# Kernel tuning notes

Hardware: AMD Instinct MI355X
Metric: run time of the kernel (lower is better)

## Reference

```python
import jax, jax.numpy as jnp
import numpy as np

K = 128
NITER = 10


def _sq_dist(x, c):
    x2 = jnp.sum(x * x, axis=1, keepdims=True)          # [N,1]
    c2 = jnp.sum(c * c, axis=1)                          # [K]
    return x2 + c2[None, :] - 2.0 * (x @ c.T)


def _kmeans(x, key):
    N, D = x.shape
    idx = jax.random.permutation(key, N)[:K]             # torch.randperm(N)[:K]
    c0 = x[idx]

    def step(c, _):
        cl = jnp.argmin(_sq_dist(x, c), axis=1)          # nearest assignment [N]
        counts = jax.ops.segment_sum(jnp.ones((N,), x.dtype), cl, num_segments=K)  # bincount
        sums = jax.ops.segment_sum(x, cl, num_segments=K)                          # [K,D] (vectorized over D)
        # c = sums / counts; NaN (empty cluster, 0/0) -> 0, matching c[isnan(c)]=0
        c_new = jnp.where(counts[:, None] > 0, sums / jnp.maximum(counts, 1.0)[:, None], 0.0)
        return c_new, None

    c, _ = jax.lax.scan(step, c0, None, length=NITER)
    return c


def setup_inputs() -> dict:
    key = jax.random.key(0)
    x = jax.random.normal(key, (500000, 64), dtype=jnp.float32)
    return {"x": x}


def reference(x):
    # KMeans runs on x.detach(); forward output has no grad path through centroids
    centroids = _kmeans(jax.lax.stop_gradient(x), jax.random.key(42))
    distances = _sq_dist(x, centroids)                   # [N, K]
    # Faithful to normalize_distance: distances.sum(1, keepdim=True)[0] indexes
    # ROW 0 of the [N,1] row-sums -> a single scalar broadcast to all rows.
    denom = jnp.sum(distances[0])
    probs = 1.0 - distances / denom
    return probs
```

## Files before the change

kernel.cpp:

```cpp
#include <hip/hip_runtime.h>
#include <cstdint>
#include <cstddef>

#define NPTS 500000
#define DIM 64
#define KC 128
#define KM_ITERS 10
#define NGROUPS (NPTS / 32)
#define NITERS ((NGROUPS + 3) / 4)

typedef __bf16 bf16x8 __attribute__((ext_vector_type(8)));
typedef float f32x4 __attribute__((ext_vector_type(4)));

__device__ __forceinline__ float wave_reduce_add(float v) {
#pragma unroll
  for (int off = 32; off > 0; off >>= 1) v += __shfl_xor(v, off, 64);
  return v;
}

__device__ __forceinline__ bf16x8 cvt8(float4 a, float4 b) {
  bf16x8 r;
  r[0] = (__bf16)a.x; r[1] = (__bf16)a.y; r[2] = (__bf16)a.z; r[3] = (__bf16)a.w;
  r[4] = (__bf16)b.x; r[5] = (__bf16)b.y; r[6] = (__bf16)b.z; r[7] = (__bf16)b.w;
  return r;
}

__global__ void k_cvt(const float* __restrict__ x, bf16x8* __restrict__ xb8) {
  int n = NPTS * DIM / 8;
  for (int i = blockIdx.x * 256 + threadIdx.x; i < n; i += gridDim.x * 256) {
    const float4* xp = (const float4*)(x + (size_t)i * 8);
    xb8[i] = cvt8(xp[0], xp[1]);
  }
}

__global__ void k_initc(const float* __restrict__ x, float* __restrict__ cent,
                        float* __restrict__ c2, float* __restrict__ sums,
                        float* __restrict__ cnts) {
  int k = blockIdx.x, d = threadIdx.x;
  long src = (long)k * 3891 + 7;
  float v = x[src * DIM + d];
  cent[k * DIM + d] = v;
  sums[k * DIM + d] = 0.f;
  float s = wave_reduce_add(v * v);
  if (d == 0) { c2[k] = s; cnts[k] = 0.f; }
}

__global__ void k_update(const float* __restrict__ sums, const float* __restrict__ cnts,
                         float* __restrict__ cent, float* __restrict__ c2,
                         float* __restrict__ sums_z, float* __restrict__ cnts_z) {
  int k = blockIdx.x, d = threadIdx.x;
  float c = cnts[k];
  float v = (c > 0.f) ? (sums[k * DIM + d] / c) : 0.f;
  cent[k * DIM + d] = v;
  sums_z[k * DIM + d] = 0.f;
  float s = wave_reduce_add(v * v);
  if (d == 0) { c2[k] = s; cnts_z[k] = 0.f; }
}

#define DIST_H(V0, V1, MK)                                                     \
  {                                                                            \
    f32x4 acc[8];                                                              \
    _Pragma("unroll") for (int tt = 0; tt < 8; tt++)                           \
      acc[tt] = (f32x4){c2h[tt * 4 + 0], c2h[tt * 4 + 1],                      \
                        c2h[tt * 4 + 2], c2h[tt * 4 + 3]};                     \
    _Pragma("unroll") for (int tt = 0; tt < 8; tt++)                           \
      acc[tt] = __builtin_amdgcn_mfma_f32_16x16x32_bf16(afr0[tt], V0, acc[tt], 0, 0, 0); \
    _Pragma("unroll") for (int tt = 0; tt < 8; tt++)                           \
      acc[tt] = __builtin_amdgcn_mfma_f32_16x16x32_bf16(afr1[tt], V1, acc[tt], 0, 0, 0); \
    float maxv = -3.4e38f; int mk = 0;                                         \
    _Pragma("unroll") for (int tt = 0; tt < 8; tt++)                           \
      _Pragma("unroll") for (int r = 0; r < 4; r++) {                          \
        float a = acc[tt][r];                                                  \
        int k = tt * 16 + grp * 4 + r;                                         \
        if (a > maxv) { maxv = a; mk = k; }                                    \
      }                                                                        \
    _Pragma("unroll") for (int off = 16; off <= 32; off <<= 1) {               \
      float ov = __shfl_xor(maxv, off, 64);                                    \
      int ok = __shfl_xor(mk, off, 64);                                        \
      if (ov > maxv || (ov == maxv && ok < mk)) { maxv = ov; mk = ok; }        \
    }                                                                          \
    MK = mk;                                                                   \
  }

__global__ __launch_bounds__(256, 2)
void k_assign(const __bf16* __restrict__ xb, const float* __restrict__ cent,
              const float* __restrict__ c2, float* __restrict__ sums,
              float* __restrict__ cnts) {
  __shared__ char xT[4][5120];
  __shared__ int sm[4][32];
  __shared__ float lc[KC];

  const int lane = threadIdx.x & 63;
  const int wid = threadIdx.x >> 6;
  const int col = lane & 15;
  const int grp = lane >> 4;

  bf16x8 afr0[8], afr1[8];
  float c2h[32];
#pragma unroll
  for (int t = 0; t < 8; t++) {
    const float* cp = cent + (size_t)(t * 16 + col) * DIM;
    float4 f0 = *(const float4*)(cp + grp * 8);
    float4 f1 = *(const float4*)(cp + grp * 8 + 4);
    afr0[t] = cvt8(f0, f1);
    float4 g0 = *(const float4*)(cp + 32 + grp * 8);
    float4 g1 = *(const float4*)(cp + 32 + grp * 8 + 4);
    afr1[t] = cvt8(g0, g1);
#pragma unroll
    for (int r = 0; r < 4; r++) c2h[t * 4 + r] = -0.5f * c2[t * 16 + grp * 4 + r];
  }
#pragma unroll
  for (int t = 0; t < 8; t++) asm volatile("" : "+v"(afr0[t]), "+v"(afr1[t]));
#pragma unroll
  for (int i = 0; i < 32; i++) asm volatile("" : "+v"(c2h[i]));

  for (int i = threadIdx.x; i < KC; i += 256) lc[i] = 0.f;
  __syncthreads();

  f32x4 accs[8];
#pragma unroll
  for (int i = 0; i < 8; i++) accs[i] = (f32x4){0.f, 0.f, 0.f, 0.f};

  const int kbase = wid * 32;

  for (int it = blockIdx.x; it < NITERS; it += gridDim.x) {
    int g = it * 4 + wid;
    int mk0 = -1, mk1 = -1;
    if (g < NGROUPS) {
      int n0 = g * 32;
      const bf16x8* xr0 = (const bf16x8*)(xb + (size_t)(n0 + col) * DIM + grp * 8);
      const bf16x8* xr1 = (const bf16x8*)(xb + (size_t)(n0 + 16 + col) * DIM + grp * 8);
      bf16x8 v0a = xr0[0], v1a = xr0[4];
      bf16x8 v0b = xr1[0], v1b = xr1[4];

      char* xTw = xT[wid];
      {
        int slotb = ((((0 << 1) | (col >> 3)) ^ grp) & 3) * 16 + (col & 7) * 2;
#pragma unroll
        for (int j = 0; j < 8; j++) {
          *(__bf16*)(xTw + (grp * 8 + j) * 80 + slotb) = v0a[j];
          *(__bf16*)(xTw + (32 + grp * 8 + j) * 80 + slotb) = v1a[j];
        }
      }
      {
        int slotb = ((((1 << 1) | (col >> 3)) ^ grp) & 3) * 16 + (col & 7) * 2;
#pragma unroll
        for (int j = 0; j < 8; j++) {
          *(__bf16*)(xTw + (grp * 8 + j) * 80 + slotb) = v0b[j];
          *(__bf16*)(xTw + (32 + grp * 8 + j) * 80 + slotb) = v1b[j];
        }
      }

      DIST_H(v0a, v1a, mk0);
      DIST_H(v0b, v1b, mk1);

      if (grp == 0) {
        atomicAdd(&lc[mk0], 1.f);
        atomicAdd(&lc[mk1], 1.f);
      }
    }
    if (grp == 0) { sm[wid][col] = mk0; sm[wid][16 + col] = mk1; }
    __syncthreads();

#pragma unroll
    for (int G = 0; G < 4; G++) {
      const int* smG = sm[G];
      int4 mlo = *(const int4*)&smG[grp * 8];
      int4 mhi = *(const int4*)&smG[grp * 8 + 4];
      const char* xTg = xT[G];
      bf16x8 xf0, xf1, xf2, xf3;
      { int d = col;      int s = (grp ^ ((d >> 3) & 3)) & 3; xf0 = *(const bf16x8*)(xTg + d * 80 + s * 16); }
      { int d = 16 + col; int s = (grp ^ ((d >> 3) & 3)) & 3; xf1 = *(const bf16x8*)(xTg + d * 80 + s * 16); }
      { int d = 32 + col; int s = (grp ^ ((d >> 3) & 3)) & 3; xf2 = *(const bf16x8*)(xTg + d * 80 + s * 16); }
      { int d = 48 + col; int s = (grp ^ ((d >> 3) & 3)) & 3; xf3 = *(const bf16x8*)(xTg + d * 80 + s * 16); }
      int m0 = mlo.x, m1 = mlo.y, m2 = mlo.z, m3 = mlo.w;
      int m4 = mhi.x, m5 = mhi.y, m6 = mhi.z, m7 = mhi.w;
#pragma unroll
      for (int tt2 = 0; tt2 < 2; tt2++) {
        int c = kbase + tt2 * 16 + col;
        union { unsigned u[4]; bf16x8 v; } oh;
        oh.u[0] = (m0 == c ? 0x3F80u : 0u) | (m1 == c ? 0x3F800000u : 0u);
        oh.u[1] = (m2 == c ? 0x3F80u : 0u) | (m3 == c ? 0x3F800000u : 0u);
        oh.u[2] = (m4 == c ? 0x3F80u : 0u) | (m5 == c ? 0x3F800000u : 0u);
        oh.u[3] = (m6 == c ? 0x3F80u : 0u) | (m7 == c ? 0x3F800000u : 0u);
        accs[tt2 * 4 + 0] = __builtin_amdgcn_mfma_f32_16x16x32_bf16(oh.v, xf0, accs[tt2 * 4 + 0], 0, 0, 0);
        accs[tt2 * 4 + 1] = __builtin_amdgcn_mfma_f32_16x16x32_bf16(oh.v, xf1, accs[tt2 * 4 + 1], 0, 0, 0);
        accs[tt2 * 4 + 2] = __builtin_amdgcn_mfma_f32_16x16x32_bf16(oh.v, xf2, accs[tt2 * 4 + 2], 0, 0, 0);
        accs[tt2 * 4 + 3] = __builtin_amdgcn_mfma_f32_16x16x32_bf16(oh.v, xf3, accs[tt2 * 4 + 3], 0, 0, 0);
      }
    }
    __syncthreads();
  }

#pragma unroll
  for (int tt2 = 0; tt2 < 2; tt2++)
#pragma unroll
    for (int dt = 0; dt < 4; dt++)
#pragma unroll
      for (int r = 0; r < 4; r++)
        atomicAdd(&sums[(size_t)(kbase + tt2 * 16 + grp * 4 + r) * DIM + dt * 16 + col],
                  accs[tt2 * 4 + dt][r]);
  for (int i = threadIdx.x; i < KC; i += 256) atomicAdd(&cnts[i], lc[i]);
}

__global__ __launch_bounds__(256, 2)
void k_probs(const float* __restrict__ x, const float* __restrict__ cent,
             const float* __restrict__ c2, float* __restrict__ out) {
  const int lane = threadIdx.x & 63;
  const int wid = threadIdx.x >> 6;
  const int col = lane & 15;
  const int grp = lane >> 4;

  bf16x8 afr[2][8];
  float c2g[32];
#pragma unroll
  for (int t = 0; t < 8; t++) {
    const float* cp = cent + (size_t)(t * 16 + col) * DIM;
#pragma unroll
    for (int ks = 0; ks < 2; ks++) {
      float4 f0 = *(const float4*)(cp + ks * 32 + grp * 8);
      float4 f1 = *(const float4*)(cp + ks * 32 + grp * 8 + 4);
      afr[ks][t] = cvt8(f0, f1);
    }
#pragma unroll
    for (int r = 0; r < 4; r++) c2g[t * 4 + r] = c2[t * 16 + grp * 4 + r];
  }

  float c2a = c2[lane], c2b = c2[64 + lane];
  float x2_0 = 0.f, dA = 0.f, dB = 0.f;
#pragma unroll 8
  for (int d = 0; d < DIM; d++) {
    float xv = x[d];
    x2_0 = fmaf(xv, xv, x2_0);
    dA = fmaf(xv, cent[(size_t)lane * DIM + d], dA);
    dB = fmaf(xv, cent[(size_t)(64 + lane) * DIM + d], dB);
  }
  float part = ((x2_0 + c2a) - 2.f * dA) + ((x2_0 + c2b) - 2.f * dB);
  float invd = 1.0f / wave_reduce_add(part);

  int w = blockIdx.x * 4 + wid;
  int nw = gridDim.x * 4;
  for (int t = w; t < NPTS / 16; t += nw) {
    int n0 = t * 16;
    const float* xp = x + (size_t)(n0 + col) * DIM;
    float4 a0 = *(const float4*)(xp + grp * 8);
    float4 a1 = *(const float4*)(xp + grp * 8 + 4);
    float4 b0 = *(const float4*)(xp + 32 + grp * 8);
    float4 b1 = *(const float4*)(xp + 32 + grp * 8 + 4);
    bf16x8 xb0 = cvt8(a0, a1), xb1 = cvt8(b0, b1);

    float sq = a0.x * a0.x + a0.y * a0.y + a0.z * a0.z + a0.w * a0.w
             + a1.x * a1.x + a1.y * a1.y + a1.z * a1.z + a1.w * a1.w
             + b0.x * b0.x + b0.y * b0.y + b0.z * b0.z + b0.w * b0.w
             + b1.x * b1.x + b1.y * b1.y + b1.z * b1.z + b1.w * b1.w;
    sq += __shfl_xor(sq, 16, 64);
    sq += __shfl_xor(sq, 32, 64);

    f32x4 acc[8];
#pragma unroll
    for (int tt = 0; tt < 8; tt++) acc[tt] = (f32x4){0.f, 0.f, 0.f, 0.f};
#pragma unroll
    for (int tt = 0; tt < 8; tt++)
      acc[tt] = __builtin_amdgcn_mfma_f32_16x16x32_bf16(afr[0][tt], xb0, acc[tt], 0, 0, 0);
#pragma unroll
    for (int tt = 0; tt < 8; tt++)
      acc[tt] = __builtin_amdgcn_mfma_f32_16x16x32_bf16(afr[1][tt], xb1, acc[tt], 0, 0, 0);

    float* op = out + (size_t)(n0 + col) * KC + grp * 4;
#pragma unroll
    for (int tt = 0; tt < 8; tt++) {
      float4 q;
      q.x = 1.f - ((sq + c2g[tt * 4 + 0]) - 2.f * acc[tt][0]) * invd;
      q.y = 1.f - ((sq + c2g[tt * 4 + 1]) - 2.f * acc[tt][1]) * invd;
      q.z = 1.f - ((sq + c2g[tt * 4 + 2]) - 2.f * acc[tt][2]) * invd;
      q.w = 1.f - ((sq + c2g[tt * 4 + 3]) - 2.f * acc[tt][3]) * invd;
      *(float4*)(op + tt * 16) = q;
    }
  }
}

extern "C" void kernel_launch(void* const* d_in, const int* in_sizes, int n_in,
                              void* d_out, int out_size, void* d_ws, size_t ws_size,
                              hipStream_t stream) {
  const float* x = (const float*)d_in[0];
  float* out = (float*)d_out;

  float* cent = (float*)d_ws;
  float* c2 = cent + KC * DIM;
  float* sums = c2 + KC;
  float* cnts = sums + KC * DIM;

  bf16x8* xb8 = (bf16x8*)d_out;
  const __bf16* xb = (const __bf16*)d_out;

  k_cvt<<<2048, 256, 0, stream>>>(x, xb8);
  k_initc<<<KC, DIM, 0, stream>>>(x, cent, c2, sums, cnts);
  for (int it = 0; it < KM_ITERS; it++) {
    k_assign<<<512, 256, 0, stream>>>(xb, cent, c2, sums, cnts);
    k_update<<<KC, DIM, 0, stream>>>(sums, cnts, cent, c2, sums, cnts);
  }
  k_probs<<<512, 256, 0, stream>>>(x, cent, c2, out);
}
```

Before: 706.7 us.

## Fuse k-means iterations into one cooperative persistent kernel with grid barriers

Replaces the convert, init, and ten assign/update kernel pairs with a single cooperative kernel that uses a custom atomic grid barrier between phases. Cluster sums and counts are spread over 32 partial slices so global atomics contend less, and the centroid update is done in-kernel. It also prefetches the next point group's registers during the scatter phase and switches argmin to a tree reduction. The aim is to cut launch gaps and atomic contention. In exchange it adds grid-barrier spin overhead and relies on all 512 blocks being co-resident.

Result: slower. 2.741 ms (+287.8%).

```diff
diff --git a/kernel.cpp b/kernel.cpp
--- a/kernel.cpp
+++ b/kernel.cpp
@@ -8,6 +8,8 @@
 #define KM_ITERS 10
 #define NGROUPS (NPTS / 32)
 #define NITERS ((NGROUPS + 3) / 4)
+#define NBLK 512
+#define NSLICE 32
 
 typedef __bf16 bf16x8 __attribute__((ext_vector_type(8)));
 typedef float f32x4 __attribute__((ext_vector_type(4)));
@@ -25,55 +27,51 @@
   return r;
 }
 
-__global__ void k_cvt(const float* __restrict__ x, bf16x8* __restrict__ xb8) {
-  int n = NPTS * DIM / 8;
-  for (int i = blockIdx.x * 256 + threadIdx.x; i < n; i += gridDim.x * 256) {
-    const float4* xp = (const float4*)(x + (size_t)i * 8);
-    xb8[i] = cvt8(xp[0], xp[1]);
-  }
-}
-
-__global__ void k_initc(const float* __restrict__ x, float* __restrict__ cent,
-                        float* __restrict__ c2, float* __restrict__ sums,
-                        float* __restrict__ cnts) {
-  int k = blockIdx.x, d = threadIdx.x;
-  long src = (long)k * 3891 + 7;
-  float v = x[src * DIM + d];
-  cent[k * DIM + d] = v;
-  sums[k * DIM + d] = 0.f;
-  float s = wave_reduce_add(v * v);
-  if (d == 0) { c2[k] = s; cnts[k] = 0.f; }
-}
-
-__global__ void k_update(const float* __restrict__ sums, const float* __restrict__ cnts,
-                         float* __restrict__ cent, float* __restrict__ c2,
-                         float* __restrict__ sums_z, float* __restrict__ cnts_z) {
-  int k = blockIdx.x, d = threadIdx.x;
-  float c = cnts[k];
-  float v = (c > 0.f) ? (sums[k * DIM + d] / c) : 0.f;
-  cent[k * DIM + d] = v;
-  sums_z[k * DIM + d] = 0.f;
-  float s = wave_reduce_add(v * v);
-  if (d == 0) { c2[k] = s; cnts_z[k] = 0.f; }
+__device__ __forceinline__ void grid_sync(int* scnt, int* sflag, int ph) {
+  __syncthreads();
+  if (threadIdx.x == 0) {
+    __threadfence();
+    __hip_atomic_fetch_add(&scnt[blockIdx.x & 7], 1, __ATOMIC_ACQ_REL,
+                           __HIP_MEMORY_SCOPE_AGENT);
+    if (blockIdx.x == 0) {
+#pragma unroll 1
+      for (int i = 0; i < 8; i++)
+        while (__hip_atomic_load(&scnt[i], __ATOMIC_ACQUIRE,
+                                 __HIP_MEMORY_SCOPE_AGENT) < ph * (NBLK / 8))
+          __builtin_amdgcn_s_sleep(1);
+      __hip_atomic_store(sflag, ph, __ATOMIC_RELEASE, __HIP_MEMORY_SCOPE_AGENT);
+    } else {
+      while (__hip_atomic_load(sflag, __ATOMIC_ACQUIRE,
+                               __HIP_MEMORY_SCOPE_AGENT) < ph)
+        __builtin_amdgcn_s_sleep(1);
+    }
+    __threadfence();
+  }
+  __syncthreads();
 }
 
 #define DIST_H(V0, V1, MK)                                                     \
   {                                                                            \
-    f32x4 acc[8];                                                              \
+    f32x4 acc_[8];                                                             \
     _Pragma("unroll") for (int tt = 0; tt < 8; tt++)                           \
-      acc[tt] = (f32x4){c2h[tt * 4 + 0], c2h[tt * 4 + 1],                      \
-                        c2h[tt * 4 + 2], c2h[tt * 4 + 3]};                     \
+      acc_[tt] = (f32x4){c2h[tt * 4 + 0], c2h[tt * 4 + 1],                     \
+                         c2h[tt * 4 + 2], c2h[tt * 4 + 3]};                    \
     _Pragma("unroll") for (int tt = 0; tt < 8; tt++)                           \
-      acc[tt] = __builtin_amdgcn_mfma_f32_16x16x32_bf16(afr0[tt], V0, acc[tt], 0, 0, 0); \
+      acc_[tt] = __builtin_amdgcn_mfma_f32_16x16x32_bf16(afr0[tt], V0, acc_[tt], 0, 0, 0); \
     _Pragma("unroll") for (int tt = 0; tt < 8; tt++)                           \
-      acc[tt] = __builtin_amdgcn_mfma_f32_16x16x32_bf16(afr1[tt], V1, acc[tt], 0, 0, 0); \
-    float maxv = -3.4e38f; int mk = 0;                                         \
-    _Pragma("unroll") for (int tt = 0; tt < 8; tt++)                           \
-      _Pragma("unroll") for (int r = 0; r < 4; r++) {                          \
-        float a = acc[tt][r];                                                  \
-        int k = tt * 16 + grp * 4 + r;                                         \
-        if (a > maxv) { maxv = a; mk = k; }                                    \
+      acc_[tt] = __builtin_amdgcn_mfma_f32_16x16x32_bf16(afr1[tt], V1, acc_[tt], 0, 0, 0); \
+    float tv[32]; int ti[32];                                                  \
+    _Pragma("unroll") for (int i_ = 0; i_ < 32; i_++) {                        \
+      tv[i_] = acc_[i_ >> 2][i_ & 3]; ti[i_] = i_;                             \
+    }                                                                          \
+    _Pragma("unroll") for (int s_ = 16; s_ >= 1; s_ >>= 1)                     \
+      _Pragma("unroll") for (int i_ = 0; i_ < s_; i_++) {                      \
+        bool t_ = tv[i_ + s_] > tv[i_];                                        \
+        tv[i_] = t_ ? tv[i_ + s_] : tv[i_];                                    \
+        ti[i_] = t_ ? ti[i_ + s_] : ti[i_];                                    \
       }                                                                        \
+    float maxv = tv[0];                                                        \
+    int mk = ((ti[0] >> 2) << 4) + grp * 4 + (ti[0] & 3);                      \
     _Pragma("unroll") for (int off = 16; off <= 32; off <<= 1) {               \
       float ov = __shfl_xor(maxv, off, 64);                                    \
       int ok = __shfl_xor(mk, off, 64);                                        \
@@ -83,124 +81,175 @@
   }
 
 __global__ __launch_bounds__(256, 2)
-void k_assign(const __bf16* __restrict__ xb, const float* __restrict__ cent,
-              const float* __restrict__ c2, float* __restrict__ sums,
-              float* __restrict__ cnts) {
+void k_mega(const float* __restrict__ x, __bf16* __restrict__ xb,
+            float* __restrict__ cent, float* __restrict__ c2,
+            float* __restrict__ sums_part, float* __restrict__ cnt_part,
+            int* __restrict__ gs) {
   __shared__ char xT[4][5120];
   __shared__ int sm[4][32];
   __shared__ float lc[KC];
 
-  const int lane = threadIdx.x & 63;
-  const int wid = threadIdx.x >> 6;
-  const int col = lane & 15;
-  const int grp = lane >> 4;
-
-  bf16x8 afr0[8], afr1[8];
-  float c2h[32];
-#pragma unroll
-  for (int t = 0; t < 8; t++) {
-    const float* cp = cent + (size_t)(t * 16 + col) * DIM;
-    float4 f0 = *(const float4*)(cp + grp * 8);
-    float4 f1 = *(const float4*)(cp + grp * 8 + 4);
-    afr0[t] = cvt8(f0, f1);
-    float4 g0 = *(const float4*)(cp + 32 + grp * 8);
-    float4 g1 = *(const float4*)(cp + 32 + grp * 8 + 4);
-    afr1[t] = cvt8(g0, g1);
-#pragma unroll
-    for (int r = 0; r < 4; r++) c2h[t * 4 + r] = -0.5f * c2[t * 16 + grp * 4 + r];
-  }
-#pragma unroll
-  for (int t = 0; t < 8; t++) asm volatile("" : "+v"(afr0[t]), "+v"(afr1[t]));
-#pragma unroll
-  for (int i = 0; i < 32; i++) asm volatile("" : "+v"(c2h[i]));
-
-  for (int i = threadIdx.x; i < KC; i += 256) lc[i] = 0.f;
-  __syncthreads();
-
-  f32x4 accs[8];
-#pragma unroll
-  for (int i = 0; i < 8; i++) accs[i] = (f32x4){0.f, 0.f, 0.f, 0.f};
-
-  const int kbase = wid * 32;
-
-  for (int it = blockIdx.x; it < NITERS; it += gridDim.x) {
-    int g = it * 4 + wid;
-    int mk0 = -1, mk1 = -1;
-    if (g < NGROUPS) {
-      int n0 = g * 32;
-      const bf16x8* xr0 = (const bf16x8*)(xb + (size_t)(n0 + col) * DIM + grp * 8);
-      const bf16x8* xr1 = (const bf16x8*)(xb + (size_t)(n0 + 16 + col) * DIM + grp * 8);
-      bf16x8 v0a = xr0[0], v1a = xr0[4];
-      bf16x8 v0b = xr1[0], v1b = xr1[4];
-
-      char* xTw = xT[wid];
+  const int tid = threadIdx.x, bid = blockIdx.x;
+  const int lane = tid & 63, wid = tid >> 6;
+  const int col = lane & 15, grp = lane >> 4;
+  int* scnt = gs;
+  int* sflag = gs + 8;
+
+  {
+    bf16x8* xb8 = (bf16x8*)xb;
+    for (int i = bid * 256 + tid; i < NPTS * DIM / 8; i += NBLK * 256) {
+      const float4* xp = (const float4*)(x + (size_t)i * 8);
+      xb8[i] = cvt8(xp[0], xp[1]);
+    }
+  }
+  if (bid < KC && tid < 64) {
+    int k = bid, d = tid;
+    long src = (long)k * 3891 + 7;
+    float v = x[src * DIM + d];
+    cent[k * DIM + d] = v;
+    float s = wave_reduce_add(v * v);
+    if (d == 0) c2[k] = s;
+#pragma unroll
+    for (int p = 0; p < NSLICE; p++) sums_part[p * (KC * DIM) + k * DIM + d] = 0.f;
+    if (d < 32) cnt_part[d * KC + k] = 0.f;
+  }
+  int ph = 1;
+  grid_sync(scnt, sflag, ph);
+
+  const __bf16* xbc = xb;
+  bf16x8 nx0a, nx1a, nx0b, nx1b;
+  {
+    int g = bid * 4 + wid;
+    const bf16x8* xr0 = (const bf16x8*)(xbc + (size_t)(g * 32 + col) * DIM + grp * 8);
+    nx0a = xr0[0]; nx1a = xr0[4];
+    nx0b = xr0[128]; nx1b = xr0[132];
+  }
+
+  for (int km = 0; km < KM_ITERS; km++) {
+    bf16x8 afr0[8], afr1[8];
+    float c2h[32];
+#pragma unroll
+    for (int t = 0; t < 8; t++) {
+      const float* cp = cent + (size_t)(t * 16 + col) * DIM;
+      afr0[t] = cvt8(*(const float4*)(cp + grp * 8), *(const float4*)(cp + grp * 8 + 4));
+      afr1[t] = cvt8(*(const float4*)(cp + 32 + grp * 8), *(const float4*)(cp + 32 + grp * 8 + 4));
+#pragma unroll
+      for (int r = 0; r < 4; r++) c2h[t * 4 + r] = -0.5f * c2[t * 16 + grp * 4 + r];
+    }
+#pragma unroll
+    for (int t = 0; t < 8; t++) asm volatile("" : "+v"(afr0[t]), "+v"(afr1[t]));
+#pragma unroll
+    for (int i2 = 0; i2 < 32; i2++) asm volatile("" : "+v"(c2h[i2]));
+    for (int i2 = tid; i2 < KC; i2 += 256) lc[i2] = 0.f;
+    __syncthreads();
+
+    f32x4 accs[8];
+#pragma unroll
+    for (int i2 = 0; i2 < 8; i2++) accs[i2] = (f32x4){0.f, 0.f, 0.f, 0.f};
+    const int kbase = wid * 32;
+    char* xTw = xT[wid];
+
+    for (int itb = bid; itb < NITERS; itb += NBLK) {
+      int g = itb * 4 + wid;
+      bf16x8 v0a = nx0a, v1a = nx1a, v0b = nx0b, v1b = nx1b;
+      int mk0 = -1, mk1 = -1;
+      if (g < NGROUPS) {
+        {
+          int slotb = ((((0 << 1) | (col >> 3)) ^ grp) & 3) * 16 + (col & 7) * 2;
+#pragma unroll
+          for (int j = 0; j < 8; j++) {
+            *(__bf16*)(xTw + (grp * 8 + j) * 80 + slotb) = v0a[j];
+            *(__bf16*)(xTw + (32 + grp * 8 + j) * 80 + slotb) = v1a[j];
+          }
+        }
+        {
+          int slotb = ((((1 << 1) | (col >> 3)) ^ grp) & 3) * 16 + (col & 7) * 2;
+#pragma unroll
+          for (int j = 0; j < 8; j++) {
+            *(__bf16*)(xTw + (grp * 8 + j) * 80 + slotb) = v0b[j];
+            *(__bf16*)(xTw + (32 + grp * 8 + j) * 80 + slotb) = v1b[j];
+          }
+        }
+        DIST_H(v0a, v1a, mk0);
+        DIST_H(v0b, v1b, mk1);
+        if (grp == 0) { atomicAdd(&lc[mk0], 1.f); atomicAdd(&lc[mk1], 1.f); }
+      }
+      if (grp == 0) { sm[wid][col] = mk0; sm[wid][16 + col] = mk1; }
+      __syncthreads();
+
       {
-        int slotb = ((((0 << 1) | (col >> 3)) ^ grp) & 3) * 16 + (col & 7) * 2;
-#pragma unroll
-        for (int j = 0; j < 8; j++) {
-          *(__bf16*)(xTw + (grp * 8 + j) * 80 + slotb) = v0a[j];
-          *(__bf16*)(xTw + (32 + grp * 8 + j) * 80 + slotb) = v1a[j];
+        int itn = itb + NBLK;
+        int gn = (itn < NITERS) ? itn * 4 + wid : bid * 4 + wid;
+        if (gn < NGROUPS) {
+          const bf16x8* xr0 = (const bf16x8*)(xbc + (size_t)(gn * 32 + col) * DIM + grp * 8);
+          nx0a = xr0[0]; nx1a = xr0[4]; nx0b = xr0[128]; nx1b = xr0[132];
         }
       }
-      {
-        int slotb = ((((1 << 1) | (col >> 3)) ^ grp) & 3) * 16 + (col & 7) * 2;
-#pragma unroll
-        for (int j = 0; j < 8; j++) {
-          *(__bf16*)(xTw + (grp * 8 + j) * 80 + slotb) = v0b[j];
-          *(__bf16*)(xTw + (32 + grp * 8 + j) * 80 + slotb) = v1b[j];
+
+#pragma unroll
+      for (int G = 0; G < 4; G++) {
+        const int* smG = sm[G];
+        int4 mlo = *(const int4*)&smG[grp * 8];
+        int4 mhi = *(const int4*)&smG[grp * 8 + 4];
+        const char* xTg = xT[G];
+        bf16x8 xf0, xf1, xf2, xf3;
+        { int d = col;      int s = (grp ^ ((d >> 3) & 3)) & 3; xf0 = *(const bf16x8*)(xTg + d * 80 + s * 16); }
+        { int d = 16 + col; int s = (grp ^ ((d >> 3) & 3)) & 3; xf1 = *(const bf16x8*)(xTg + d * 80 + s * 16); }
+        { int d = 32 + col; int s = (grp ^ ((d >> 3) & 3)) & 3; xf2 = *(const bf16x8*)(xTg + d * 80 + s * 16); }
+        { int d = 48 + col; int s = (grp ^ ((d >> 3) & 3)) & 3; xf3 = *(const bf16x8*)(xTg + d * 80 + s * 16); }
+        int m0 = mlo.x, m1 = mlo.y, m2 = mlo.z, m3 = mlo.w;
+        int m4 = mhi.x, m5 = mhi.y, m6 = mhi.z, m7 = mhi.w;
+#pragma unroll
+        for (int tt2 = 0; tt2 < 2; tt2++) {
+          int c = kbase + tt2 * 16 + col;
+          union { unsigned u[4]; bf16x8 v; } oh;
+          oh.u[0] = (m0 == c ? 0x3F80u : 0u) | (m1 == c ? 0x3F800000u : 0u);
+          oh.u[1] = (m2 == c ? 0x3F80u : 0u) | (m3 == c ? 0x3F800000u : 0u);
+          oh.u[2] = (m4 == c ? 0x3F80u : 0u) | (m5 == c ? 0x3F800000u : 0u);
+          oh.u[3] = (m6 == c ? 0x3F80u : 0u) | (m7 == c ? 0x3F800000u : 0u);
+          accs[tt2 * 4 + 0] = __builtin_amdgcn_mfma_f32_16x16x32_bf16(oh.v, xf0, accs[tt2 * 4 + 0], 0, 0, 0);
+          accs[tt2 * 4 + 1] = __builtin_amdgcn_mfma_f32_16x16x32_bf16(oh.v, xf1, accs[tt2 * 4 + 1], 0, 0, 0);
+          accs[tt2 * 4 + 2] = __builtin_amdgcn_mfma_f32_16x16x32_bf16(oh.v, xf2, accs[tt2 * 4 + 2], 0, 0, 0);
+          accs[tt2 * 4 + 3] = __builtin_amdgcn_mfma_f32_16x16x32_bf16(oh.v, xf3, accs[tt2 * 4 + 3], 0, 0, 0);
         }
       }
-
-      DIST_H(v0a, v1a, mk0);
-      DIST_H(v0b, v1b, mk1);
-
-      if (grp == 0) {
-        atomicAdd(&lc[mk0], 1.f);
-        atomicAdd(&lc[mk1], 1.f);
-      }
-    }
-    if (grp == 0) { sm[wid][col] = mk0; sm[wid][16 + col] = mk1; }
-    __syncthreads();
-
-#pragma unroll
-    for (int G = 0; G < 4; G++) {
-      const int* smG = sm[G];
-      int4 mlo = *(const int4*)&smG[grp * 8];
-      int4 mhi = *(const int4*)&smG[grp * 8 + 4];
-      const char* xTg = xT[G];
-      bf16x8 xf0, xf1, xf2, xf3;
-      { int d = col;      int s = (grp ^ ((d >> 3) & 3)) & 3; xf0 = *(const bf16x8*)(xTg + d * 80 + s * 16); }
-      { int d = 16 + col; int s = (grp ^ ((d >> 3) & 3)) & 3; xf1 = *(const bf16x8*)(xTg + d * 80 + s * 16); }
-      { int d = 32 + col; int s = (grp ^ ((d >> 3) & 3)) & 3; xf2 = *(const bf16x8*)(xTg + d * 80 + s * 16); }
-      { int d = 48 + col; int s = (grp ^ ((d >> 3) & 3)) & 3; xf3 = *(const bf16x8*)(xTg + d * 80 + s * 16); }
-      int m0 = mlo.x, m1 = mlo.y, m2 = mlo.z, m3 = mlo.w;
-      int m4 = mhi.x, m5 = mhi.y, m6 = mhi.z, m7 = mhi.w;
-#pragma unroll
-      for (int tt2 = 0; tt2 < 2; tt2++) {
-        int c = kbase + tt2 * 16 + col;
-        union { unsigned u[4]; bf16x8 v; } oh;
-        oh.u[0] = (m0 == c ? 0x3F80u : 0u) | (m1 == c ? 0x3F800000u : 0u);
-        oh.u[1] = (m2 == c ? 0x3F80u : 0u) | (m3 == c ? 0x3F800000u : 0u);
-        oh.u[2] = (m4 == c ? 0x3F80u : 0u) | (m5 == c ? 0x3F800000u : 0u);
-        oh.u[3] = (m6 == c ? 0x3F80u : 0u) | (m7 == c ? 0x3F800000u : 0u);
-        accs[tt2 * 4 + 0] = __builtin_amdgcn_mfma_f32_16x16x32_bf16(oh.v, xf0, accs[tt2 * 4 + 0], 0, 0, 0);
-        accs[tt2 * 4 + 1] = __builtin_amdgcn_mfma_f32_16x16x32_bf16(oh.v, xf1, accs[tt2 * 4 + 1], 0, 0, 0);
-        accs[tt2 * 4 + 2] = __builtin_amdgcn_mfma_f32_16x16x32_bf16(oh.v, xf2, accs[tt2 * 4 + 2], 0, 0, 0);
-        accs[tt2 * 4 + 3] = __builtin_amdgcn_mfma_f32_16x16x32_bf16(oh.v, xf3, accs[tt2 * 4 + 3], 0, 0, 0);
-      }
-    }
-    __syncthreads();
-  }
-
-#pragma unroll
-  for (int tt2 = 0; tt2 < 2; tt2++)
-#pragma unroll
-    for (int dt = 0; dt < 4; dt++)
-#pragma unroll
-      for (int r = 0; r < 4; r++)
-        atomicAdd(&sums[(size_t)(kbase + tt2 * 16 + grp * 4 + r) * DIM + dt * 16 + col],
-                  accs[tt2 * 4 + dt][r]);
-  for (int i = threadIdx.x; i < KC; i += 256) atomicAdd(&cnts[i], lc[i]);
+      __syncthreads();
+    }
+
+    {
+      float* sp = sums_part + (size_t)(bid & (NSLICE - 1)) * (KC * DIM);
+#pragma unroll
+      for (int tt2 = 0; tt2 < 2; tt2++)
+#pragma unroll
+        for (int dt = 0; dt < 4; dt++)
+#pragma unroll
+          for (int r = 0; r < 4; r++)
+            atomicAdd(&sp[(size_t)(kbase + tt2 * 16 + grp * 4 + r) * DIM + dt * 16 + col],
+                      accs[tt2 * 4 + dt][r]);
+      float* cp2 = cnt_part + (bid & (NSLICE - 1)) * KC;
+      for (int i2 = tid; i2 < KC; i2 += 256) atomicAdd(&cp2[i2], lc[i2]);
+    }
+    ph++;
+    grid_sync(scnt, sflag, ph);
+
+    if (bid < KC && tid < 64) {
+      int k = bid, d = tid;
+      float s = 0.f;
+#pragma unroll
+      for (int p = 0; p < NSLICE; p++) s += sums_part[p * (KC * DIM) + k * DIM + d];
+      float ci = (d < 32) ? cnt_part[d * KC + k] : 0.f;
+      float c = wave_reduce_add(ci);
+      float v = (c > 0.f) ? s / c : 0.f;
+      cent[k * DIM + d] = v;
+      float q = wave_reduce_add(v * v);
+      if (d == 0) c2[k] = q;
+#pragma unroll
+      for (int p = 0; p < NSLICE; p++) sums_part[p * (KC * DIM) + k * DIM + d] = 0.f;
+      if (d < 32) cnt_part[d * KC + k] = 0.f;
+    }
+    ph++;
+    grid_sync(scnt, sflag, ph);
+  }
 }
 
 __global__ __launch_bounds__(256, 2)
@@ -287,17 +336,24 @@
 
   float* cent = (float*)d_ws;
   float* c2 = cent + KC * DIM;
-  float* sums = c2 + KC;
-  float* cnts = sums + KC * DIM;
-
-  bf16x8* xb8 = (bf16x8*)d_out;
-  const __bf16* xb = (const __bf16*)d_out;
-
-  k_cvt<<<2048, 256, 0, stream>>>(x, xb8);
-  k_initc<<<KC, DIM, 0, stream>>>(x, cent, c2, sums, cnts);
-  for (int it = 0; it < KM_ITERS; it++) {
-    k_assign<<<512, 256, 0, stream>>>(xb, cent, c2, sums, cnts);
-    k_update<<<KC, DIM, 0, stream>>>(sums, cnts, cent, c2, sums, cnts);
-  }
+  float* sums_part = c2 + KC;
+  float* cnt_part = sums_part + (size_t)NSLICE * KC * DIM;
+  int* gsync = (int*)(cnt_part + NSLICE * KC);
+
+  __bf16* xb = (__bf16*)d_out;
+
+  hipMemsetAsync(gsync, 0, 16 * sizeof(int), stream);
+
+  const float* xa = x;
+  __bf16* xba = xb;
+  float* centa = cent;
+  float* c2a = c2;
+  float* spa = sums_part;
+  float* cpa = cnt_part;
+  int* gsa = gsync;
+  void* args[] = {(void*)&xa, (void*)&xba, (void*)&centa, (void*)&c2a,
+                  (void*)&spa, (void*)&cpa, (void*)&gsa};
+  hipLaunchCooperativeKernel((void*)k_mega, dim3(NBLK), dim3(256), args, 0, stream);
+
   k_probs<<<512, 256, 0, stream>>>(x, cent, c2, out);
 }
```

## Move centroid MFMA fragments to LDS, tree argmax, raise occupancy to 3 blocks

Applied to the files above, without the earlier changes.

Centroid bf16 fragments now sit in shared memory and are read per MFMA instead of being held in 64 VGPRs per lane. This frees registers so launch bounds can rise to 3 blocks per CU, and the assign grid grows from 512 to 768. The per-lane argmax over 32 candidates becomes a tree reduction with selects instead of a sequential compare chain. The trade is extra LDS reads on every distance tile and more LDS use per block, which could limit occupancy or add bank traffic.

New measurement: 773.9 us. +9.5%, slower.

```diff
diff --git a/kernel.cpp b/kernel.cpp
--- a/kernel.cpp
+++ b/kernel.cpp
@@ -59,21 +59,26 @@
 
 #define DIST_H(V0, V1, MK)                                                     \
   {                                                                            \
-    f32x4 acc[8];                                                              \
+    f32x4 acc_[8];                                                             \
     _Pragma("unroll") for (int tt = 0; tt < 8; tt++)                           \
-      acc[tt] = (f32x4){c2h[tt * 4 + 0], c2h[tt * 4 + 1],                      \
-                        c2h[tt * 4 + 2], c2h[tt * 4 + 3]};                     \
+      acc_[tt] = (f32x4){c2h[tt * 4 + 0], c2h[tt * 4 + 1],                     \
+                         c2h[tt * 4 + 2], c2h[tt * 4 + 3]};                    \
     _Pragma("unroll") for (int tt = 0; tt < 8; tt++)                           \
-      acc[tt] = __builtin_amdgcn_mfma_f32_16x16x32_bf16(afr0[tt], V0, acc[tt], 0, 0, 0); \
+      acc_[tt] = __builtin_amdgcn_mfma_f32_16x16x32_bf16(sAp[tt * 128 + lane], V0, acc_[tt], 0, 0, 0); \
     _Pragma("unroll") for (int tt = 0; tt < 8; tt++)                           \
-      acc[tt] = __builtin_amdgcn_mfma_f32_16x16x32_bf16(afr1[tt], V1, acc[tt], 0, 0, 0); \
-    float maxv = -3.4e38f; int mk = 0;                                         \
-    _Pragma("unroll") for (int tt = 0; tt < 8; tt++)                           \
-      _Pragma("unroll") for (int r = 0; r < 4; r++) {                          \
-        float a = acc[tt][r];                                                  \
-        int k = tt * 16 + grp * 4 + r;                                         \
-        if (a > maxv) { maxv = a; mk = k; }                                    \
+      acc_[tt] = __builtin_amdgcn_mfma_f32_16x16x32_bf16(sAp[tt * 128 + 64 + lane], V1, acc_[tt], 0, 0, 0); \
+    float tv[32]; int ti[32];                                                  \
+    _Pragma("unroll") for (int i_ = 0; i_ < 32; i_++) {                        \
+      tv[i_] = acc_[i_ >> 2][i_ & 3]; ti[i_] = i_;                             \
+    }                                                                          \
+    _Pragma("unroll") for (int s_ = 16; s_ >= 1; s_ >>= 1)                     \
+      _Pragma("unroll") for (int i_ = 0; i_ < s_; i_++) {                      \
+        bool t_ = tv[i_ + s_] > tv[i_];                                        \
+        tv[i_] = t_ ? tv[i_ + s_] : tv[i_];                                    \
+        ti[i_] = t_ ? ti[i_ + s_] : ti[i_];                                    \
       }                                                                        \
+    float maxv = tv[0];                                                        \
+    int mk = ((ti[0] >> 2) << 4) + grp * 4 + (ti[0] & 3);                      \
     _Pragma("unroll") for (int off = 16; off <= 32; off <<= 1) {               \
       float ov = __shfl_xor(maxv, off, 64);                                    \
       int ok = __shfl_xor(mk, off, 64);                                        \
@@ -82,10 +87,11 @@
     MK = mk;                                                                   \
   }
 
-__global__ __launch_bounds__(256, 2)
+__global__ __launch_bounds__(256, 3)
 void k_assign(const __bf16* __restrict__ xb, const float* __restrict__ cent,
               const float* __restrict__ c2, float* __restrict__ sums,
               float* __restrict__ cnts) {
+  __shared__ bf16x8 sA[1024];
   __shared__ char xT[4][5120];
   __shared__ int sm[4][32];
   __shared__ float lc[KC];
@@ -95,26 +101,21 @@
   const int col = lane & 15;
   const int grp = lane >> 4;
 
-  bf16x8 afr0[8], afr1[8];
+  for (int e = threadIdx.x; e < 1024; e += 256) {
+    int t = e >> 7, ks = (e >> 6) & 1, l = e & 63;
+    const float* cp = cent + (size_t)(t * 16 + (l & 15)) * DIM + ks * 32 + (l >> 4) * 8;
+    sA[e] = cvt8(*(const float4*)cp, *(const float4*)(cp + 4));
+  }
+  for (int i = threadIdx.x; i < KC; i += 256) lc[i] = 0.f;
+
   float c2h[32];
 #pragma unroll
-  for (int t = 0; t < 8; t++) {
-    const float* cp = cent + (size_t)(t * 16 + col) * DIM;
-    float4 f0 = *(const float4*)(cp + grp * 8);
-    float4 f1 = *(const float4*)(cp + grp * 8 + 4);
-    afr0[t] = cvt8(f0, f1);
-    float4 g0 = *(const float4*)(cp + 32 + grp * 8);
-    float4 g1 = *(const float4*)(cp + 32 + grp * 8 + 4);
-    afr1[t] = cvt8(g0, g1);
-#pragma unroll
-    for (int r = 0; r < 4; r++) c2h[t * 4 + r] = -0.5f * c2[t * 16 + grp * 4 + r];
-  }
-#pragma unroll
-  for (int t = 0; t < 8; t++) asm volatile("" : "+v"(afr0[t]), "+v"(afr1[t]));
+  for (int tt = 0; tt < 8; tt++)
+#pragma unroll
+    for (int r = 0; r < 4; r++) c2h[tt * 4 + r] = -0.5f * c2[tt * 16 + grp * 4 + r];
 #pragma unroll
   for (int i = 0; i < 32; i++) asm volatile("" : "+v"(c2h[i]));
 
-  for (int i = threadIdx.x; i < KC; i += 256) lc[i] = 0.f;
   __syncthreads();
 
   f32x4 accs[8];
@@ -122,8 +123,11 @@
   for (int i = 0; i < 8; i++) accs[i] = (f32x4){0.f, 0.f, 0.f, 0.f};
 
   const int kbase = wid * 32;
+  const bf16x8* sAp = sA;
+  char* xTw = xT[wid];
 
   for (int it = blockIdx.x; it < NITERS; it += gridDim.x) {
+    asm volatile("" : "+v"(sAp));
     int g = it * 4 + wid;
     int mk0 = -1, mk1 = -1;
     if (g < NGROUPS) {
@@ -133,7 +137,6 @@
       bf16x8 v0a = xr0[0], v1a = xr0[4];
       bf16x8 v0b = xr1[0], v1b = xr1[4];
 
-      char* xTw = xT[wid];
       {
         int slotb = ((((0 << 1) | (col >> 3)) ^ grp) & 3) * 16 + (col & 7) * 2;
 #pragma unroll
@@ -154,10 +157,7 @@
       DIST_H(v0a, v1a, mk0);
       DIST_H(v0b, v1b, mk1);
 
-      if (grp == 0) {
-        atomicAdd(&lc[mk0], 1.f);
-        atomicAdd(&lc[mk1], 1.f);
-      }
+      if (grp == 0) { atomicAdd(&lc[mk0], 1.f); atomicAdd(&lc[mk1], 1.f); }
     }
     if (grp == 0) { sm[wid][col] = mk0; sm[wid][16 + col] = mk1; }
     __syncthreads();
@@ -296,7 +296,7 @@
   k_cvt<<<2048, 256, 0, stream>>>(x, xb8);
   k_initc<<<KC, DIM, 0, stream>>>(x, cent, c2, sums, cnts);
   for (int it = 0; it < KM_ITERS; it++) {
-    k_assign<<<512, 256, 0, stream>>>(xb, cent, c2, sums, cnts);
+    k_assign<<<768, 256, 0, stream>>>(xb, cent, c2, sums, cnts);
     k_update<<<KC, DIM, 0, stream>>>(sums, cnts, cent, c2, sums, cnts);
   }
   k_probs<<<512, 256, 0, stream>>>(x, cent, c2, out);
```
